# Optimization experiments

Hardware: AMD Instinct MI355X
Metric: run time of the kernel (lower is better)

Reference implementation:

```python
import jax, jax.numpy as jnp
import numpy as np


def setup_inputs() -> dict:
    key = jax.random.key(0)
    k1, k2, k3, k4, k5 = jax.random.split(key, 5)
    F_total, T, D, K = 256, 576, 1408, 144  # frames, in_token_num, num_features, out_token_num
    return {
        "image_embeds": jax.random.normal(k1, (F_total, T, D), jnp.float32),
        "pre_w": jax.random.normal(k2, (1, D), jnp.float32) * 0.02,
        "pre_b": jax.random.normal(k3, (1,), jnp.float32) * 0.02,
        "trans_weight": jax.random.normal(k4, (T, T), jnp.float32) * 0.02,
        "trans_bias": jax.random.normal(k5, (T,), jnp.float32) * 0.02,
        "n_frames": 32,
        "out_token_num": K,
    }


def reference(image_embeds, pre_w, pre_b, trans_weight, trans_bias, n_frames, out_token_num):
    # image_embeds: [F_total, T, D]
    F_total, T, D = image_embeds.shape
    # pre_proj: Linear(D, 1) -> per-token scalar score, [F_total, T]
    s = jnp.einsum('ftd,d->ft', image_embeds, pre_w[0]) + pre_b[0]
    # [F,1,T] @ [T,T] + bias -> squeeze(1) == [F,T] @ W + b
    logits = s @ trans_weight + trans_bias                    # [F_total, T]
    scores = jax.nn.softmax(logits, axis=-1)                  # [F_total, T]
    # top-k via descending argsort, then restore ascending token order
    idx = jnp.sort(jnp.argsort(-scores, axis=-1)[:, :out_token_num], axis=-1)  # [F_total, K]
    sel = jnp.take_along_axis(image_embeds, idx[:, :, None], axis=1)           # [F_total, K, D]
    # torch returns a list of per-video tensors; with uniform n_frames this is
    # equivalently a stacked [n_videos, n_frames, K, D] array.
    n_videos = F_total // n_frames
    return sel.reshape(n_videos, n_frames, out_token_num, D)
```

## Files before the change

### kernel.cpp

```cpp
#include <hip/hip_runtime.h>
#include <stdint.h>

typedef float f4 __attribute__((ext_vector_type(4)));

__device__ __forceinline__ double dot4d(f4 a, f4 b) {
    return (double)a.x * (double)b.x + (double)a.y * (double)b.y
         + (double)a.z * (double)b.z + (double)a.w * (double)b.w;
}

template <int T, int D, int K>
__global__ __launch_bounds__(1024)
void fused_v4_kernel(const float* __restrict__ x,
                     const float* __restrict__ pre_w,
                     const float* __restrict__ pre_b,
                     const float* __restrict__ W,
                     const float* __restrict__ bias,
                     float* __restrict__ out) {
    constexpr int N4   = D / 4;
    constexpr int NJ   = N4 / 16;
    constexpr int NGRP = 64;
    constexpr int RPG  = T / NGRP;
    constexpr int NW   = (T + 31) / 32;
    constexpr int RFULL = N4 / 64;
    constexpr int RREM  = N4 - RFULL * 64;
    static_assert(NJ == 22 && RPG * NGRP == T, "shape assumptions");

    __shared__ f4       w_sh[N4];
    __shared__ double   s_sh[T];
    __shared__ double   lg[T];
    __shared__ unsigned flags[NW];
    __shared__ int      sel[K];

    const int f    = blockIdx.x;
    const int tid  = threadIdx.x;
    const int sub  = tid & 15;
    const int gid  = tid >> 4;
    const int wave = tid >> 6;
    const int lane = tid & 63;

    for (int i = tid; i < N4; i += 1024) w_sh[i] = ((const f4*)pre_w)[i];
    if (tid < NW) flags[tid] = 0u;
    __syncthreads();

    const double pb = (double)pre_b[0];
    for (int m = 0; m < RPG; ++m) {
        const int r = gid + NGRP * m;
        const f4* xr = (const f4*)(x + ((size_t)f * T + r) * D);
        double a0 = 0, a1 = 0, a2 = 0, a3 = 0;
        #pragma unroll 2
        for (int j = 0; j < 16; j += 4) {
            f4 v0 = xr[sub + 16 * (j + 0)];
            f4 v1 = xr[sub + 16 * (j + 1)];
            f4 v2 = xr[sub + 16 * (j + 2)];
            f4 v3 = xr[sub + 16 * (j + 3)];
            a0 += dot4d(v0, w_sh[sub + 16 * (j + 0)]);
            a1 += dot4d(v1, w_sh[sub + 16 * (j + 1)]);
            a2 += dot4d(v2, w_sh[sub + 16 * (j + 2)]);
            a3 += dot4d(v3, w_sh[sub + 16 * (j + 3)]);
        }
        {
            f4 v0 = xr[sub + 16 * 16];
            f4 v1 = xr[sub + 16 * 17];
            f4 v2 = xr[sub + 16 * 18];
            f4 v3 = xr[sub + 16 * 19];
            f4 v4 = xr[sub + 16 * 20];
            f4 v5 = xr[sub + 16 * 21];
            a0 += dot4d(v0, w_sh[sub + 16 * 16]);
            a1 += dot4d(v1, w_sh[sub + 16 * 17]);
            a2 += dot4d(v2, w_sh[sub + 16 * 18]);
            a3 += dot4d(v3, w_sh[sub + 16 * 19]);
            a0 += dot4d(v4, w_sh[sub + 16 * 20]);
            a1 += dot4d(v5, w_sh[sub + 16 * 21]);
        }
        double s = (a0 + a1) + (a2 + a3);
        s += __shfl_down(s, 8, 16);
        s += __shfl_down(s, 4, 16);
        s += __shfl_down(s, 2, 16);
        s += __shfl_down(s, 1, 16);
        if (sub == 0) s_sh[r] = s + pb;
    }
    __syncthreads();

    if (tid < T) {
        const float* Wc = W + tid;
        double acc[16];
        #pragma unroll
        for (int u = 0; u < 16; ++u) acc[u] = 0.0;
        for (int tp = 0; tp < T; tp += 16) {
            #pragma unroll
            for (int u = 0; u < 16; ++u)
                acc[u] += s_sh[tp + u] * (double)Wc[(size_t)(tp + u) * T];
        }
        double r0 = (acc[0] + acc[1]) + (acc[2] + acc[3]);
        double r1 = (acc[4] + acc[5]) + (acc[6] + acc[7]);
        double r2 = (acc[8] + acc[9]) + (acc[10] + acc[11]);
        double r3 = (acc[12] + acc[13]) + (acc[14] + acc[15]);
        lg[tid] = ((r0 + r1) + (r2 + r3)) + (double)bias[tid];
    }
    __syncthreads();

    if (tid < T) {
        const double v = lg[tid];
        int rank = 0;
        #pragma unroll 8
        for (int tp = 0; tp < T; ++tp) {
            double u = lg[tp];
            rank += (u > v) || (u == v && tp < tid);
        }
        if (rank < K) atomicOr(&flags[tid >> 5], 1u << (tid & 31));
    }
    __syncthreads();

    if (tid < T) {
        if ((flags[tid >> 5] >> (tid & 31)) & 1u) {
            int pos = __popc(flags[tid >> 5] & ((1u << (tid & 31)) - 1u));
            for (int u2 = 0; u2 < (tid >> 5); ++u2) pos += __popc(flags[u2]);
            sel[pos] = tid;
        }
    }
    __syncthreads();

    for (int k2 = wave; k2 < K; k2 += 16) {
        const int t = sel[k2];
        const f4* src = (const f4*)(x + ((size_t)f * T + t) * D);
        f4*       dst = (f4*)(out + ((size_t)f * K + k2) * D);
        f4 v0 = src[lane + 64 * 0];
        f4 v1 = src[lane + 64 * 1];
        f4 v2 = src[lane + 64 * 2];
        f4 v3 = src[lane + 64 * 3];
        f4 v4 = src[lane + 64 * 4];
        __builtin_nontemporal_store(v0, &dst[lane + 64 * 0]);
        __builtin_nontemporal_store(v1, &dst[lane + 64 * 1]);
        __builtin_nontemporal_store(v2, &dst[lane + 64 * 2]);
        __builtin_nontemporal_store(v3, &dst[lane + 64 * 3]);
        __builtin_nontemporal_store(v4, &dst[lane + 64 * 4]);
        if (lane < RREM) {
            f4 v5 = src[lane + 64 * RFULL];
            __builtin_nontemporal_store(v5, &dst[lane + 64 * RFULL]);
        }
    }
}

__global__ __launch_bounds__(1024)
void fused_select_kernel(const float* __restrict__ x,
                         const float* __restrict__ pre_w,
                         const float* __restrict__ pre_b,
                         const float* __restrict__ W,
                         const float* __restrict__ bias,
                         float* __restrict__ out,
                         int T, int D, int K) {
    __shared__ double   s_sh[1024];
    __shared__ double   lg[1024];
    __shared__ unsigned flags[32];
    __shared__ int      sel[576];

    const int f    = blockIdx.x;
    const int tid  = threadIdx.x;
    const int wave = tid >> 6;
    const int lane = tid & 63;
    const int nw   = blockDim.x >> 6;
    const int n4   = D >> 2;

    const f4* wv = (const f4*)pre_w;
    for (int t = wave; t < T; t += nw) {
        const f4* xr = (const f4*)(x + ((size_t)f * T + t) * D);
        double acc = 0.0;
        for (int p = lane; p < n4; p += 64) acc += dot4d(xr[p], wv[p]);
#pragma unroll
        for (int off = 32; off > 0; off >>= 1) acc += __shfl_down(acc, off);
        if (lane == 0) s_sh[t] = acc + (double)pre_b[0];
    }
    if (tid < 32) flags[tid] = 0u;
    __syncthreads();

    if (tid < T) {
        const float* Wc = W + tid;
        double a0 = 0, a1 = 0, a2 = 0, a3 = 0;
        int tp = 0;
        for (; tp + 4 <= T; tp += 4) {
            a0 += s_sh[tp + 0] * (double)Wc[(size_t)(tp + 0) * T];
            a1 += s_sh[tp + 1] * (double)Wc[(size_t)(tp + 1) * T];
            a2 += s_sh[tp + 2] * (double)Wc[(size_t)(tp + 2) * T];
            a3 += s_sh[tp + 3] * (double)Wc[(size_t)(tp + 3) * T];
        }
        for (; tp < T; ++tp) a0 += s_sh[tp] * (double)Wc[(size_t)tp * T];
        lg[tid] = ((a0 + a1) + (a2 + a3)) + (double)bias[tid];
    }
    __syncthreads();
    if (tid < T) {
        const double v = lg[tid];
        int rank = 0;
        for (int tp = 0; tp < T; ++tp) {
            double u = lg[tp];
            rank += (u > v) || (u == v && tp < tid);
        }
        if (rank < K) atomicOr(&flags[tid >> 5], 1u << (tid & 31));
    }
    __syncthreads();
    if (tid < T) {
        if ((flags[tid >> 5] >> (tid & 31)) & 1u) {
            int pos = __popc(flags[tid >> 5] & ((1u << (tid & 31)) - 1u));
            for (int u2 = 0; u2 < (tid >> 5); ++u2) pos += __popc(flags[u2]);
            sel[pos] = tid;
        }
    }
    __syncthreads();
    for (int k2 = wave; k2 < K; k2 += nw) {
        int t = sel[k2];
        const f4* src = (const f4*)(x + ((size_t)f * T + t) * D);
        f4*       dst = (f4*)(out + ((size_t)f * K + k2) * D);
        for (int p = lane; p < n4; p += 64)
            __builtin_nontemporal_store(src[p], &dst[p]);
    }
}

extern "C" void kernel_launch(void* const* d_in, const int* in_sizes, int n_in,
                              void* d_out, int out_size, void* d_ws, size_t ws_size,
                              hipStream_t stream) {
    const float* x     = (const float*)d_in[0];
    const float* pre_w = (const float*)d_in[1];
    const float* pre_b = (const float*)d_in[2];
    const float* W     = (const float*)d_in[3];
    const float* bias  = (const float*)d_in[4];
    float* outp = (float*)d_out;

    const int D = in_sizes[1];
    const int T = in_sizes[4];
    const int F = in_sizes[0] / (T * D);
    const int K = out_size / (F * D);

    if (T == 576 && D == 1408 && K == 144) {
        fused_v4_kernel<576, 1408, 144><<<F, 1024, 0, stream>>>(
            x, pre_w, pre_b, W, bias, outp);
    } else {
        fused_select_kernel<<<F, 1024, 0, stream>>>(x, pre_w, pre_b, W, bias,
                                                    outp, T, D, K);
    }
}
```

Baseline: 253.7 us.

## Split fused per-frame kernel into score, select and gather kernels

Replaces the single 256-block fused kernel with three launches: a scoring kernel over 64-row chunks (2304 blocks), a per-frame select kernel writing top-k indices to workspace, and a gather kernel with one wave per output row. The aim is to fill all compute units during the bandwidth-heavy score and gather phases, since 256 blocks of 1024 threads underuse the GPU. The cost is two extra launches, a workspace round-trip for scores and indices, and losing the cache locality that came from the fused gather rereading frame rows.

New measurement: 264.6 us. 4.3% more time.

```diff
diff --git a/kernel.cpp b/kernel.cpp
--- a/kernel.cpp
+++ b/kernel.cpp
@@ -8,44 +8,28 @@
          + (double)a.z * (double)b.z + (double)a.w * (double)b.w;
 }
 
-template <int T, int D, int K>
-__global__ __launch_bounds__(1024)
-void fused_v4_kernel(const float* __restrict__ x,
-                     const float* __restrict__ pre_w,
-                     const float* __restrict__ pre_b,
-                     const float* __restrict__ W,
-                     const float* __restrict__ bias,
-                     float* __restrict__ out) {
-    constexpr int N4   = D / 4;
-    constexpr int NJ   = N4 / 16;
-    constexpr int NGRP = 64;
-    constexpr int RPG  = T / NGRP;
-    constexpr int NW   = (T + 31) / 32;
-    constexpr int RFULL = N4 / 64;
-    constexpr int RREM  = N4 - RFULL * 64;
-    static_assert(NJ == 22 && RPG * NGRP == T, "shape assumptions");
-
-    __shared__ f4       w_sh[N4];
-    __shared__ double   s_sh[T];
-    __shared__ double   lg[T];
-    __shared__ unsigned flags[NW];
-    __shared__ int      sel[K];
-
-    const int f    = blockIdx.x;
+template <int T, int D>
+__global__ __launch_bounds__(256)
+void score_k(const float* __restrict__ x,
+             const float* __restrict__ pre_w,
+             const float* __restrict__ pre_b,
+             double* __restrict__ s) {
+    constexpr int N4 = D / 4;
+    __shared__ f4 w_sh[N4];
+
     const int tid  = threadIdx.x;
     const int sub  = tid & 15;
     const int gid  = tid >> 4;
-    const int wave = tid >> 6;
-    const int lane = tid & 63;
-
-    for (int i = tid; i < N4; i += 1024) w_sh[i] = ((const f4*)pre_w)[i];
-    if (tid < NW) flags[tid] = 0u;
+    const int base = blockIdx.x * 64;
+
+    for (int i = tid; i < N4; i += 256) w_sh[i] = ((const f4*)pre_w)[i];
     __syncthreads();
 
     const double pb = (double)pre_b[0];
-    for (int m = 0; m < RPG; ++m) {
-        const int r = gid + NGRP * m;
-        const f4* xr = (const f4*)(x + ((size_t)f * T + r) * D);
+    #pragma unroll
+    for (int m = 0; m < 4; ++m) {
+        const int r = base + gid + 16 * m;
+        const f4* xr = (const f4*)(x + (size_t)r * D);
         double a0 = 0, a1 = 0, a2 = 0, a3 = 0;
         #pragma unroll 2
         for (int j = 0; j < 16; j += 4) {
@@ -72,16 +56,34 @@
             a0 += dot4d(v4, w_sh[sub + 16 * 20]);
             a1 += dot4d(v5, w_sh[sub + 16 * 21]);
         }
-        double s = (a0 + a1) + (a2 + a3);
-        s += __shfl_down(s, 8, 16);
-        s += __shfl_down(s, 4, 16);
-        s += __shfl_down(s, 2, 16);
-        s += __shfl_down(s, 1, 16);
-        if (sub == 0) s_sh[r] = s + pb;
-    }
-    __syncthreads();
-
-    if (tid < T) {
+        double a = (a0 + a1) + (a2 + a3);
+        a += __shfl_down(a, 8, 16);
+        a += __shfl_down(a, 4, 16);
+        a += __shfl_down(a, 2, 16);
+        a += __shfl_down(a, 1, 16);
+        if (sub == 0) s[r] = a + pb;
+    }
+}
+
+template <int T, int K>
+__global__ __launch_bounds__(T)
+void select_k(const double* __restrict__ s,
+              const float* __restrict__ W,
+              const float* __restrict__ bias,
+              int* __restrict__ idx_out) {
+    constexpr int NW = (T + 31) / 32;
+    __shared__ double   s_sh[T];
+    __shared__ double   lg[T];
+    __shared__ unsigned flags[NW];
+
+    const int f   = blockIdx.x;
+    const int tid = threadIdx.x;
+
+    s_sh[tid] = s[(size_t)f * T + tid];
+    if (tid < NW) flags[tid] = 0u;
+    __syncthreads();
+
+    {
         const float* Wc = W + tid;
         double acc[16];
         #pragma unroll
@@ -99,7 +101,7 @@
     }
     __syncthreads();
 
-    if (tid < T) {
+    {
         const double v = lg[tid];
         int rank = 0;
         #pragma unroll 8
@@ -111,33 +113,44 @@
     }
     __syncthreads();
 
-    if (tid < T) {
+    {
         if ((flags[tid >> 5] >> (tid & 31)) & 1u) {
             int pos = __popc(flags[tid >> 5] & ((1u << (tid & 31)) - 1u));
             for (int u2 = 0; u2 < (tid >> 5); ++u2) pos += __popc(flags[u2]);
-            sel[pos] = tid;
-        }
-    }
-    __syncthreads();
-
-    for (int k2 = wave; k2 < K; k2 += 16) {
-        const int t = sel[k2];
-        const f4* src = (const f4*)(x + ((size_t)f * T + t) * D);
-        f4*       dst = (f4*)(out + ((size_t)f * K + k2) * D);
-        f4 v0 = src[lane + 64 * 0];
-        f4 v1 = src[lane + 64 * 1];
-        f4 v2 = src[lane + 64 * 2];
-        f4 v3 = src[lane + 64 * 3];
-        f4 v4 = src[lane + 64 * 4];
-        __builtin_nontemporal_store(v0, &dst[lane + 64 * 0]);
-        __builtin_nontemporal_store(v1, &dst[lane + 64 * 1]);
-        __builtin_nontemporal_store(v2, &dst[lane + 64 * 2]);
-        __builtin_nontemporal_store(v3, &dst[lane + 64 * 3]);
-        __builtin_nontemporal_store(v4, &dst[lane + 64 * 4]);
-        if (lane < RREM) {
-            f4 v5 = src[lane + 64 * RFULL];
-            __builtin_nontemporal_store(v5, &dst[lane + 64 * RFULL]);
-        }
+            idx_out[(size_t)f * K + pos] = tid;
+        }
+    }
+}
+
+template <int T, int D, int K>
+__global__ __launch_bounds__(256)
+void gather_k(const float* __restrict__ x,
+              const int* __restrict__ idx,
+              float* __restrict__ out) {
+    constexpr int N4 = D / 4;
+    constexpr int RFULL = N4 / 64;
+    constexpr int RREM  = N4 - RFULL * 64;
+
+    const int lane = threadIdx.x & 63;
+    const int row  = blockIdx.x * 4 + (threadIdx.x >> 6);
+    const int f    = row / K;
+    const int t    = idx[row];
+
+    const f4* src = (const f4*)(x + ((size_t)f * T + t) * D);
+    f4*       dst = (f4*)(out + (size_t)row * D);
+    f4 v0 = src[lane + 64 * 0];
+    f4 v1 = src[lane + 64 * 1];
+    f4 v2 = src[lane + 64 * 2];
+    f4 v3 = src[lane + 64 * 3];
+    f4 v4 = src[lane + 64 * 4];
+    __builtin_nontemporal_store(v0, &dst[lane + 64 * 0]);
+    __builtin_nontemporal_store(v1, &dst[lane + 64 * 1]);
+    __builtin_nontemporal_store(v2, &dst[lane + 64 * 2]);
+    __builtin_nontemporal_store(v3, &dst[lane + 64 * 3]);
+    __builtin_nontemporal_store(v4, &dst[lane + 64 * 4]);
+    if (lane < RREM) {
+        f4 v5 = src[lane + 64 * RFULL];
+        __builtin_nontemporal_store(v5, &dst[lane + 64 * RFULL]);
     }
 }
 
@@ -229,9 +242,13 @@
     const int F = in_sizes[0] / (T * D);
     const int K = out_size / (F * D);
 
-    if (T == 576 && D == 1408 && K == 144) {
-        fused_v4_kernel<576, 1408, 144><<<F, 1024, 0, stream>>>(
-            x, pre_w, pre_b, W, bias, outp);
+    if (T == 576 && D == 1408 && K == 144 && (F * T) % 64 == 0 && (F * K) % 4 == 0) {
+        double* s_buf = (double*)d_ws;
+        int*    idx   = (int*)((char*)d_ws + (size_t)F * T * sizeof(double));
+
+        score_k<576, 1408><<<(F * T) / 64, 256, 0, stream>>>(x, pre_w, pre_b, s_buf);
+        select_k<576, 144><<<F, 576, 0, stream>>>(s_buf, W, bias, idx);
+        gather_k<576, 1408, 144><<<(F * K) / 4, 256, 0, stream>>>(x, idx, outp);
     } else {
         fused_select_kernel<<<F, 1024, 0, stream>>>(x, pre_w, pre_b, W, bias,
                                                     outp, T, D, K);
```

## Overlap score computation with partial GEMV and use nontemporal loads in gather

Applied to the files above, without the earlier changes.

Splits the 576×576 score GEMV into chunks of 64 rows and interleaves each chunk with computing the next batch of per-token dot-product scores. This lets the memory-bound streaming of the embedding rows overlap with reading W, instead of running them as two separate phases. The cost is one block barrier per chunk, nine in total. The gather copy also switches its source reads to nontemporal loads to reduce cache pollution. That may lose L2 hits on rows that were just read for scoring.

Result: slower. 395.6 us (+55.9%).

```diff
diff --git a/kernel.cpp b/kernel.cpp
--- a/kernel.cpp
+++ b/kernel.cpp
@@ -10,20 +10,19 @@
 
 template <int T, int D, int K>
 __global__ __launch_bounds__(1024)
-void fused_v4_kernel(const float* __restrict__ x,
+void fused_v5_kernel(const float* __restrict__ x,
                      const float* __restrict__ pre_w,
                      const float* __restrict__ pre_b,
                      const float* __restrict__ W,
                      const float* __restrict__ bias,
                      float* __restrict__ out) {
     constexpr int N4   = D / 4;
-    constexpr int NJ   = N4 / 16;
     constexpr int NGRP = 64;
-    constexpr int RPG  = T / NGRP;
+    constexpr int NB   = T / NGRP;
     constexpr int NW   = (T + 31) / 32;
     constexpr int RFULL = N4 / 64;
     constexpr int RREM  = N4 - RFULL * 64;
-    static_assert(NJ == 22 && RPG * NGRP == T, "shape assumptions");
+    static_assert(N4 == 16 * 22 && NB * NGRP == T, "shape assumptions");
 
     __shared__ f4       w_sh[N4];
     __shared__ double   s_sh[T];
@@ -43,7 +42,8 @@
     __syncthreads();
 
     const double pb = (double)pre_b[0];
-    for (int m = 0; m < RPG; ++m) {
+
+    auto score_row = [&](int m) {
         const int r = gid + NGRP * m;
         const f4* xr = (const f4*)(x + ((size_t)f * T + r) * D);
         double a0 = 0, a1 = 0, a2 = 0, a3 = 0;
@@ -72,31 +72,39 @@
             a0 += dot4d(v4, w_sh[sub + 16 * 20]);
             a1 += dot4d(v5, w_sh[sub + 16 * 21]);
         }
-        double s = (a0 + a1) + (a2 + a3);
-        s += __shfl_down(s, 8, 16);
-        s += __shfl_down(s, 4, 16);
-        s += __shfl_down(s, 2, 16);
-        s += __shfl_down(s, 1, 16);
-        if (sub == 0) s_sh[r] = s + pb;
-    }
-    __syncthreads();
-
-    if (tid < T) {
-        const float* Wc = W + tid;
-        double acc[16];
-        #pragma unroll
-        for (int u = 0; u < 16; ++u) acc[u] = 0.0;
-        for (int tp = 0; tp < T; tp += 16) {
-            #pragma unroll
-            for (int u = 0; u < 16; ++u)
-                acc[u] += s_sh[tp + u] * (double)Wc[(size_t)(tp + u) * T];
-        }
-        double r0 = (acc[0] + acc[1]) + (acc[2] + acc[3]);
-        double r1 = (acc[4] + acc[5]) + (acc[6] + acc[7]);
-        double r2 = (acc[8] + acc[9]) + (acc[10] + acc[11]);
-        double r3 = (acc[12] + acc[13]) + (acc[14] + acc[15]);
-        lg[tid] = ((r0 + r1) + (r2 + r3)) + (double)bias[tid];
-    }
+        double a = (a0 + a1) + (a2 + a3);
+        a += __shfl_down(a, 8, 16);
+        a += __shfl_down(a, 4, 16);
+        a += __shfl_down(a, 2, 16);
+        a += __shfl_down(a, 1, 16);
+        if (sub == 0) s_sh[r] = a + pb;
+    };
+
+    double g0 = 0, g1 = 0, g2 = 0, g3 = 0;
+    const float* Wc = W + tid;
+
+    auto gemv_partial = [&](int mb) {
+        if (tid < T) {
+            const int base = NGRP * mb;
+            #pragma unroll 8
+            for (int j = 0; j < NGRP; j += 4) {
+                g0 += s_sh[base + j + 0] * (double)Wc[(size_t)(base + j + 0) * T];
+                g1 += s_sh[base + j + 1] * (double)Wc[(size_t)(base + j + 1) * T];
+                g2 += s_sh[base + j + 2] * (double)Wc[(size_t)(base + j + 2) * T];
+                g3 += s_sh[base + j + 3] * (double)Wc[(size_t)(base + j + 3) * T];
+            }
+        }
+    };
+
+    score_row(0);
+    __syncthreads();
+    for (int m = 1; m < NB; ++m) {
+        score_row(m);
+        gemv_partial(m - 1);
+        __syncthreads();
+    }
+    gemv_partial(NB - 1);
+    if (tid < T) lg[tid] = ((g0 + g1) + (g2 + g3)) + (double)bias[tid];
     __syncthreads();
 
     if (tid < T) {
@@ -124,18 +132,18 @@
         const int t = sel[k2];
         const f4* src = (const f4*)(x + ((size_t)f * T + t) * D);
         f4*       dst = (f4*)(out + ((size_t)f * K + k2) * D);
-        f4 v0 = src[lane + 64 * 0];
-        f4 v1 = src[lane + 64 * 1];
-        f4 v2 = src[lane + 64 * 2];
-        f4 v3 = src[lane + 64 * 3];
-        f4 v4 = src[lane + 64 * 4];
+        f4 v0 = __builtin_nontemporal_load(&src[lane + 64 * 0]);
+        f4 v1 = __builtin_nontemporal_load(&src[lane + 64 * 1]);
+        f4 v2 = __builtin_nontemporal_load(&src[lane + 64 * 2]);
+        f4 v3 = __builtin_nontemporal_load(&src[lane + 64 * 3]);
+        f4 v4 = __builtin_nontemporal_load(&src[lane + 64 * 4]);
         __builtin_nontemporal_store(v0, &dst[lane + 64 * 0]);
         __builtin_nontemporal_store(v1, &dst[lane + 64 * 1]);
         __builtin_nontemporal_store(v2, &dst[lane + 64 * 2]);
         __builtin_nontemporal_store(v3, &dst[lane + 64 * 3]);
         __builtin_nontemporal_store(v4, &dst[lane + 64 * 4]);
         if (lane < RREM) {
-            f4 v5 = src[lane + 64 * RFULL];
+            f4 v5 = __builtin_nontemporal_load(&src[lane + 64 * RFULL]);
             __builtin_nontemporal_store(v5, &dst[lane + 64 * RFULL]);
         }
     }
@@ -230,7 +238,7 @@
     const int K = out_size / (F * D);
 
     if (T == 576 && D == 1408 && K == 144) {
-        fused_v4_kernel<576, 1408, 144><<<F, 1024, 0, stream>>>(
+        fused_v5_kernel<576, 1408, 144><<<F, 1024, 0, stream>>>(
             x, pre_w, pre_b, W, bias, outp);
     } else {
         fused_select_kernel<<<F, 1024, 0, stream>>>(x, pre_w, pre_b, W, bias,
```
